# Performance work log

Measured on AMD Instinct MI355X. Metric: run time of the kernel, lower is better.

Reference implementation:

```python
import jax, jax.numpy as jnp
import numpy as np


def setup_inputs() -> dict:
    key = jax.random.key(0)
    ks = jax.random.split(key, 6)
    b, c, h, w = 8, 256, 48, 48
    return {
        "qry_fts": jax.random.normal(ks[0], (b, c, h, w), dtype=jnp.float32),
        "mask_fts": jax.random.normal(ks[1], (b, c, h, w), dtype=jnp.float32),
        "fts": jax.random.normal(ks[2], (b, c, h, w), dtype=jnp.float32),
        "Wq": jax.random.normal(ks[3], (c, c), dtype=jnp.float32) * (1.0 / np.sqrt(c)),
        "Wk": jax.random.normal(ks[4], (c, c), dtype=jnp.float32) * (1.0 / np.sqrt(c)),
        "Wv": jax.random.normal(ks[5], (c, c), dtype=jnp.float32) * (1.0 / np.sqrt(c)),
        "mu": jnp.full((1,), 0.5, dtype=jnp.float32),
    }


def reference(qry_fts, mask_fts, fts, Wq, Wk, Wv, mu):
    b, c, h, w = qry_fts.shape
    # flatten spatial dims to tokens: [b, N, c], N = h*w
    q_tok = qry_fts.reshape(b, c, h * w).transpose(0, 2, 1)
    m_tok = mask_fts.reshape(b, c, h * w).transpose(0, 2, 1)
    f_tok = fts.reshape(b, c, h * w).transpose(0, 2, 1)

    # torch Linear(no bias): y = x @ W^T with W [out,in]
    Q = jnp.einsum("bnc,dc->bnd", q_tok, Wq)
    K1 = jnp.einsum("bnc,dc->bnd", f_tok, Wk)
    K2 = jnp.einsum("bnc,dc->bnd", m_tok, Wk)
    V = jnp.einsum("bnc,dc->bnd", f_tok, Wv)

    A1 = jax.nn.softmax(jnp.einsum("bqd,bkd->bqk", Q, K1), axis=-1)
    A2 = jax.nn.softmax(jnp.einsum("bqd,bkd->bqk", Q, K2), axis=-1)
    A = (A1 * 0.5 + A2 * mu[0]) / (0.5 + mu[0])

    att = jnp.einsum("bqk,bkd->bqd", A, V)  # [b, N, c]
    att = att.reshape(b, h, w, c).transpose(0, 3, 1, 2)
    return qry_fts + att
```

## Files before the change

### kernel.cpp

```cpp
#include <hip/hip_runtime.h>
#include <math.h>

#define BB 8
#define CC 256
#define NTOK 2304
#define NPL 36
#define LOG2E 1.4426950408889634f
#define BIAS2 72.134752f

typedef __attribute__((ext_vector_type(4))) float f32x4;
typedef __attribute__((ext_vector_type(8))) short s16x8;
typedef __attribute__((ext_vector_type(4))) short s16x4;

__device__ inline unsigned short f2bf(float x) {
  unsigned u = __builtin_bit_cast(unsigned, x);
  return (unsigned short)((u + 0x7FFFu + ((u >> 16) & 1u)) >> 16);
}
__device__ inline float bf2f(unsigned short h) {
  return __builtin_bit_cast(float, (unsigned)h << 16);
}
__device__ inline unsigned short f2h(float x) {
  _Float16 h = (_Float16)x;
  return __builtin_bit_cast(unsigned short, h);
}

__device__ inline void async16(void* lds, const void* g) {
  __builtin_amdgcn_global_load_lds(
      (const __attribute__((address_space(1))) unsigned int*)g,
      (__attribute__((address_space(3))) unsigned int*)lds, 16, 0, 0);
}

__global__ __launch_bounds__(256)
void prep_kernel(const float* __restrict__ X0, const float* __restrict__ X1,
                 const float* __restrict__ X2, unsigned short* __restrict__ Y0,
                 unsigned short* __restrict__ Y1, unsigned short* __restrict__ Y2) {
  __shared__ float Ls[64][65];
  const int t = threadIdx.x;
  const int n0 = blockIdx.x * 64, c0 = blockIdx.y * 64;
  const int z = blockIdx.z, src = z >> 3, b = z & 7;
  const float* X = (src == 0) ? X0 : (src == 1) ? X1 : X2;
  unsigned short* Y = (src == 0) ? Y0 : (src == 1) ? Y1 : Y2;
  const float* Xb = X + (size_t)b * CC * NTOK;
  unsigned short* Yb = Y + (size_t)b * CC * NTOK;

  #pragma unroll
  for (int rr = 0; rr < 16; rr++) {
    int cl = rr * 4 + (t >> 6);
    Ls[cl][t & 63] = Xb[(size_t)(c0 + cl) * NTOK + n0 + (t & 63)];
  }
  __syncthreads();
  #pragma unroll
  for (int rr = 0; rr < 8; rr++) {
    int nl = rr * 8 + (t >> 5);
    int cl = (t & 31) * 2;
    unsigned v = (unsigned)f2h(Ls[cl][nl]) | ((unsigned)f2h(Ls[cl + 1][nl]) << 16);
    *(unsigned*)((char*)Yb + ((size_t)(n0 + nl) * CC + c0 + cl) * 2) = v;
  }
}

__global__ __launch_bounds__(256)
void wconv_kernel(const float* __restrict__ Wq, const float* __restrict__ Wk,
                  const float* __restrict__ Wv, unsigned short* __restrict__ Wqh,
                  unsigned short* __restrict__ Wkh, unsigned short* __restrict__ Wvh) {
  const float* src = (blockIdx.y == 0) ? Wq : (blockIdx.y == 1) ? Wk : Wv;
  unsigned short* dst = (blockIdx.y == 0) ? Wqh : (blockIdx.y == 1) ? Wkh : Wvh;
  int gi = (blockIdx.x * 256 + threadIdx.x) * 4;
  f32x4 v = *(const f32x4*)(src + gi);
  s16x4 o;
  #pragma unroll
  for (int i = 0; i < 4; i++) o[i] = (short)f2h(v[i]);
  *(s16x4*)(dst + gi) = o;
}

__global__ __launch_bounds__(256, 2)
void gemm_kernel(const unsigned short* __restrict__ Xtq, const unsigned short* __restrict__ Xtm,
                 const unsigned short* __restrict__ Xtf, const unsigned short* __restrict__ Wqh,
                 const unsigned short* __restrict__ Wkh, const unsigned short* __restrict__ Wvh,
                 unsigned short* __restrict__ Qw, unsigned short* __restrict__ K1w,
                 unsigned short* __restrict__ K2w, unsigned short* __restrict__ Vtw) {
  __shared__ alignas(16) char smem[32768];

  const int m = blockIdx.y;
  const unsigned short* Xt = (m == 0) ? Xtq : (m == 2) ? Xtm : Xtf;
  const unsigned short* Wh = (m == 0) ? Wqh : (m == 3) ? Wvh : Wkh;
  unsigned short* Y = (m == 0) ? Qw : (m == 1) ? K1w : (m == 2) ? K2w : Vtw;

  const int t = threadIdx.x;
  const int w = t >> 6, l = t & 63, g = l >> 4, c = l & 15;
  const int bid = blockIdx.x;
  const int b = bid & 7, nt = bid >> 3;
  const int n0w = nt * 64 + w * 16;
  const size_t bo = (size_t)b * CC * NTOK;

  const char* Xb = (const char*)(Xt + bo);
  const char* Wb = (const char*)Wh;
  char* Yb = (char*)(Y + bo);

  int koff[4], cdst[4];
  #pragma unroll
  for (int j = 0; j < 4; j++) {
    int ck = w + 4 * j;
    int row = ck * 2 + (l >> 5);
    koff[j] = row * 512 + (((l & 31) * 16) ^ ((row & 7) << 4));
    cdst[j] = ck * 1024 + l * 16;
  }
  int kxor[8];
  #pragma unroll
  for (int dc = 0; dc < 8; dc++)
    kxor[dc] = (dc * 64 + g * 16) ^ ((c & 7) << 4);

  s16x8 xa[8];
  #pragma unroll
  for (int dc = 0; dc < 8; dc++)
    xa[dc] = *(const s16x8*)(Xb + (n0w + c) * 512 + dc * 64 + g * 16);

  f32x4 acc[16];

#define STAGE_W(WB, TILE)                                            \
  do {                                                               \
    _Pragma("unroll")                                                \
    for (int j_ = 0; j_ < 4; j_++)                                   \
      async16((WB) + cdst[j_], Wb + (TILE) * 16384 + koff[j_]);      \
  } while (0)

  STAGE_W(smem, 0);
  __syncthreads();

  #pragma unroll
  for (int ph = 0; ph < 8; ph++) {
    char* cur = smem + (ph & 1) * 16384;
    if (ph < 7) STAGE_W(smem + ((ph & 1) ^ 1) * 16384, ph + 1);
    __builtin_amdgcn_s_setprio(1);
    #pragma unroll
    for (int s = 0; s < 2; s++) {
      const char* Kt = cur + (s * 16 + c) * 512;
      f32x4 sx[2] = {(f32x4){0.f, 0.f, 0.f, 0.f}, (f32x4){0.f, 0.f, 0.f, 0.f}};
      #pragma unroll
      for (int dc = 0; dc < 8; dc++) {
        s16x8 wf = *(const s16x8*)(Kt + kxor[dc]);
        sx[dc >> 2] = __builtin_amdgcn_mfma_f32_16x16x32_f16(xa[dc], wf, sx[dc >> 2], 0, 0, 0);
      }
      acc[ph * 2 + s] = sx[0] + sx[1];
    }
    __builtin_amdgcn_s_setprio(0);
    __syncthreads();
  }
#undef STAGE_W

  if (m != 3) {
    unsigned short* Ws = (unsigned short*)(smem + w * 8192);
    const float scale = (m == 0) ? LOG2E : 1.0f;
    #pragma unroll
    for (int dt = 0; dt < 16; dt++)
      #pragma unroll
      for (int j = 0; j < 4; j++)
        Ws[(g * 4 + j) * 256 + dt * 16 + c] = f2h(acc[dt][j] * scale);
    #pragma unroll
    for (int r = 0; r < 16; r++) {
      s16x4 v = *(const s16x4*)&Ws[r * 256 + l * 4];
      *(s16x4*)(Yb + (size_t)(n0w + r) * 512 + l * 8) = v;
    }
  } else {
    unsigned short* Vs = (unsigned short*)(smem + w * 8192);
    #pragma unroll
    for (int dt = 0; dt < 16; dt++) {
      s16x4 pv;
      #pragma unroll
      for (int j = 0; j < 4; j++) pv[j] = (short)f2bf(acc[dt][j]);
      *(s16x4*)&Vs[c * 20 + g * 4] = pv;
      s16x4 vv = *(const s16x4*)&Vs[(l >> 2) * 20 + (l & 3) * 4];
      *(s16x4*)(Yb + (size_t)(dt * 16 + (l >> 2)) * 4608 + (size_t)(n0w + (l & 3) * 4) * 2) = vv;
    }
  }
}

__global__ __launch_bounds__(256, 2)
void attn_kernel(const unsigned short* __restrict__ Qf, const unsigned short* __restrict__ K1,
                 const unsigned short* __restrict__ K2, const unsigned short* __restrict__ Vt,
                 unsigned short* __restrict__ pa1, unsigned short* __restrict__ pa2,
                 float* __restrict__ lb) {
  __shared__ alignas(16) char smem[77824];
  char* const kb0 = smem;
  char* const kb1 = smem + 16384;

  const int t = threadIdx.x;
  const int w = t >> 6, l = t & 63, g = l >> 4, c = l & 15;
  const int path = w >> 1, qs = w & 1;
  const int bid = blockIdx.x;
  const int b = bid & 7;
  const int r0 = bid >> 3;
  const int qt = r0 % 36, half = r0 / 36;
  const int q0 = qt * 64 + qs * 32;
  const size_t bo = (size_t)b * CC * NTOK;

  const char* Qb  = (const char*)(Qf + bo);
  const char* K1b = (const char*)(K1 + bo);
  const char* K2b = (const char*)(K2 + bo);
  const char* Vtb = (const char*)(Vt + bo);

  unsigned short* const Pe  = (unsigned short*)(smem + 65536 + w * 3072);
  unsigned short* const Pod = Pe + 768;

  int koff[2], voff[2], cdst[2];
  #pragma unroll
  for (int j = 0; j < 2; j++) {
    int ck = w + 4 * j;
    int tok = ck * 2 + (l >> 5);
    koff[j] = tok * 512 + (((l & 31) * 16) ^ ((tok & 7) << 4));
    voff[j] = (ck * 32 + (l >> 1)) * 4608 + (((l & 1) ^ ((l >> 3) & 1)) << 4);
    cdst[j] = ck * 1024 + l * 16;
  }

  int kxor[8];
  #pragma unroll
  for (int dc = 0; dc < 8; dc++)
    kxor[dc] = (dc * 64 + g * 16) ^ ((c & 7) << 4);

  s16x8 qf[2][8];
  #pragma unroll
  for (int st = 0; st < 2; st++)
    #pragma unroll
    for (int dc = 0; dc < 8; dc++)
      qf[st][dc] = *(const s16x8*)(Qb + (q0 + st * 16 + c) * 512 + dc * 64 + g * 16);

  f32x4 a0[16], a1r[16];
  #pragma unroll
  for (int dt = 0; dt < 16; dt++) {
    a0[dt]  = (f32x4){0.f, 0.f, 0.f, 0.f};
    a1r[dt] = (f32x4){0.f, 0.f, 0.f, 0.f};
  }
  float lr[2][4] = {{0.f, 0.f, 0.f, 0.f}, {0.f, 0.f, 0.f, 0.f}};

#define STAGE_K(KB, TILE)                                                  \
  do {                                                                     \
    _Pragma("unroll")                                                      \
    for (int pp_ = 0; pp_ < 2; pp_++) {                                    \
      const char* ks_ = (pp_ ? K2b : K1b) + (size_t)(TILE) * 8192;         \
      async16((KB) + pp_ * 8192 + cdst[0], ks_ + koff[0]);                 \
      async16((KB) + pp_ * 8192 + cdst[1], ks_ + koff[1]);                 \
    }                                                                      \
  } while (0)

#define STAGE_V(VB, PAIR)                                                  \
  do {                                                                     \
    _Pragma("unroll")                                                      \
    for (int h_ = 0; h_ < 2; h_++) {                                       \
      const char* vs_ = Vtb + (PAIR) * 64 + h_ * 32;                       \
      async16((VB) + h_ * 8192 + cdst[0], vs_ + voff[0]);                  \
      async16((VB) + h_ * 8192 + cdst[1], vs_ + voff[1]);                  \
    }                                                                      \
  } while (0)

  const int tb = half * 72;
  const int pb = half * 36;

  STAGE_K(kb0, tb);
  STAGE_V(smem + 32768, pb);
  __syncthreads();

  for (int p = 0; p < NPL; p++) {
    char* vcur = smem + 32768 + (p & 1) * 16384;
    char* vnxt = smem + 32768 + ((p & 1) ^ 1) * 16384;

    STAGE_K(kb1, tb + 2 * p + 1);
    {
      const char* Kt = kb0 + path * 8192 + c * 512;
      f32x4 s0 = (f32x4){0.f, 0.f, 0.f, 0.f};
      f32x4 s1 = (f32x4){0.f, 0.f, 0.f, 0.f};
      __builtin_amdgcn_s_setprio(1);
      #pragma unroll
      for (int dc = 0; dc < 8; dc++) {
        s16x8 kf = *(const s16x8*)(Kt + kxor[dc]);
        s0 = __builtin_amdgcn_mfma_f32_16x16x32_f16(qf[0][dc], kf, s0, 0, 0, 0);
        s1 = __builtin_amdgcn_mfma_f32_16x16x32_f16(qf[1][dc], kf, s1, 0, 0, 0);
      }
      __builtin_amdgcn_s_setprio(0);
      #pragma unroll
      for (int j = 0; j < 4; j++) {
        float pv = exp2f(s0[j] - BIAS2);
        lr[0][j] += pv;
        Pe[(g * 4 + j) * 24 + c] = f2bf(pv);
        float pw = exp2f(s1[j] - BIAS2);
        lr[1][j] += pw;
        Pe[(16 + g * 4 + j) * 24 + c] = f2bf(pw);
      }
    }
    __syncthreads();

    if (p + 1 < NPL) {
      STAGE_K(kb0, tb + 2 * p + 2);
      STAGE_V(vnxt, pb + p + 1);
    }
    {
      const char* Kt = kb1 + path * 8192 + c * 512;
      f32x4 s0 = (f32x4){0.f, 0.f, 0.f, 0.f};
      f32x4 s1 = (f32x4){0.f, 0.f, 0.f, 0.f};
      __builtin_amdgcn_s_setprio(1);
      #pragma unroll
      for (int dc = 0; dc < 8; dc++) {
        s16x8 kf = *(const s16x8*)(Kt + kxor[dc]);
        s0 = __builtin_amdgcn_mfma_f32_16x16x32_f16(qf[0][dc], kf, s0, 0, 0, 0);
        s1 = __builtin_amdgcn_mfma_f32_16x16x32_f16(qf[1][dc], kf, s1, 0, 0, 0);
      }
      __builtin_amdgcn_s_setprio(0);
      #pragma unroll
      for (int j = 0; j < 4; j++) {
        float pv = exp2f(s0[j] - BIAS2);
        lr[0][j] += pv;
        Pod[(g * 4 + j) * 24 + c] = f2bf(pv);
        float pw = exp2f(s1[j] - BIAS2);
        lr[1][j] += pw;
        Pod[(16 + g * 4 + j) * 24 + c] = f2bf(pw);
      }
    }
    {
      s16x8 pa0 = *(const s16x8*)(((g < 2) ? Pe : Pod) + (c) * 24 + (g & 1) * 8);
      s16x8 pa1 = *(const s16x8*)(((g < 2) ? Pe : Pod) + (16 + c) * 24 + (g & 1) * 8);
      const char* vbase = vcur + ((g >= 2) ? 8192 : 0) + c * 32 +
                          ((((g & 1) ^ ((c >> 2) & 1))) << 4);
      __builtin_amdgcn_s_setprio(1);
      #pragma unroll
      for (int dt = 0; dt < 16; dt++) {
        s16x8 vf = *(const s16x8*)(vbase + dt * 512);
        a0[dt]  = __builtin_amdgcn_mfma_f32_16x16x32_bf16(pa0, vf, a0[dt], 0, 0, 0);
        a1r[dt] = __builtin_amdgcn_mfma_f32_16x16x32_bf16(pa1, vf, a1r[dt], 0, 0, 0);
      }
      __builtin_amdgcn_s_setprio(0);
    }
    __syncthreads();
  }
#undef STAGE_K
#undef STAGE_V

  #pragma unroll
  for (int st = 0; st < 2; st++)
    #pragma unroll
    for (int j = 0; j < 4; j++) {
      #pragma unroll
      for (int off = 1; off < 16; off <<= 1)
        lr[st][j] += __shfl_xor(lr[st][j], off);
    }
  const int pqidx = (half * 8 + b) * 36 + qt;
  if (c == 0) {
    #pragma unroll
    for (int st = 0; st < 2; st++)
      #pragma unroll
      for (int j = 0; j < 4; j++)
        lb[path * 36864 + pqidx * 64 + qs * 32 + st * 16 + g * 4 + j] = lr[st][j];
  }

  unsigned short* const pdst = (path ? pa2 : pa1) + (size_t)pqidx * 16384;
  float* Ws = (float*)(smem + w * 4352);
  const int q = l & 15, ds = l >> 4;
  #pragma unroll
  for (int st = 0; st < 2; st++) {
    const f32x4* ap = st ? a1r : a0;
    #pragma unroll
    for (int ch = 0; ch < 4; ch++) {
      #pragma unroll
      for (int dtp = 0; dtp < 4; dtp++) {
        const int dt = ch * 4 + dtp;
        #pragma unroll
        for (int j = 0; j < 4; j++)
          Ws[(g * 4 + j) * 68 + dtp * 16 + c] = ap[dt][j];
      }
      #pragma unroll
      for (int i = 0; i < 16; i++) {
        int d = ch * 64 + i * 4 + ds;
        pdst[d * 64 + qs * 32 + st * 16 + q] = f2bf(Ws[q * 68 + i * 4 + ds]);
      }
    }
  }
}

__global__ __launch_bounds__(256)
void combine_kernel(const unsigned short* __restrict__ pa1, const unsigned short* __restrict__ pa2,
                    const float* __restrict__ lb, const float* __restrict__ qry,
                    const float* __restrict__ mup, float* __restrict__ out) {
  const int bid = blockIdx.x;
  const int b = bid & 7, qt = bid >> 3;
  const int t = threadIdx.x;
  const int q = t & 63, dr = t >> 6;
  const size_t bo = (size_t)b * CC * NTOK;
  const int q0 = qt * 64;

  const int i0 = (0 * 8 + b) * 36 + qt;
  const int i1 = (1 * 8 + b) * 36 + qt;
  float l1 = lb[i0 * 64 + q] + lb[i1 * 64 + q];
  float l2 = lb[36864 + i0 * 64 + q] + lb[36864 + i1 * 64 + q];
  const float mu = mup[0];
  const float w1 = 0.5f / (0.5f + mu) / l1;
  const float w2 = mu / (0.5f + mu) / l2;

  const unsigned short* p10 = pa1 + (size_t)i0 * 16384;
  const unsigned short* p11 = pa1 + (size_t)i1 * 16384;
  const unsigned short* p20 = pa2 + (size_t)i0 * 16384;
  const unsigned short* p21 = pa2 + (size_t)i1 * 16384;

  #pragma unroll
  for (int i = 0; i < 64; i++) {
    int d = dr * 64 + i;
    int off = d * 64 + q;
    float av1 = bf2f(p10[off]) + bf2f(p11[off]);
    float av2 = bf2f(p20[off]) + bf2f(p21[off]);
    size_t gi = bo + (size_t)d * NTOK + q0 + q;
    out[gi] = qry[gi] + av1 * w1 + av2 * w2;
  }
}

extern "C" void kernel_launch(void* const* d_in, const int* in_sizes, int n_in,
                              void* d_out, int out_size, void* d_ws, size_t ws_size,
                              hipStream_t stream) {
  const float* qry  = (const float*)d_in[0];
  const float* mask = (const float*)d_in[1];
  const float* fts  = (const float*)d_in[2];
  const float* Wq   = (const float*)d_in[3];
  const float* Wk   = (const float*)d_in[4];
  const float* Wv   = (const float*)d_in[5];
  const float* mu   = (const float*)d_in[6];
  float* out = (float*)d_out;

  const size_t SZ = (size_t)BB * CC * NTOK;
  unsigned short* base = (unsigned short*)d_ws;
  unsigned short* PA1 = base;
  unsigned short* PA2 = base + 9437184;
  float*          LB  = (float*)(base + 18874368);
  unsigned short* Xtq = base;
  unsigned short* Xtm = base + SZ;
  unsigned short* Xtf = base + 2 * SZ;
  unsigned short* Qw  = base + 19169280;
  unsigned short* K1w = Qw + SZ;
  unsigned short* K2w = Qw + 2 * SZ;
  unsigned short* Vtw = Qw + 3 * SZ;
  unsigned short* Wqh = Qw + 4 * SZ;
  unsigned short* Wkh = Wqh + CC * CC;
  unsigned short* Wvh = Wkh + CC * CC;

  prep_kernel<<<dim3(NTOK / 64, CC / 64, 24), 256, 0, stream>>>(qry, mask, fts, Xtq, Xtm, Xtf);
  wconv_kernel<<<dim3(64, 3), 256, 0, stream>>>(Wq, Wk, Wv, Wqh, Wkh, Wvh);

  const int GG = BB * (NTOK / 64);
  gemm_kernel<<<dim3(GG, 4), 256, 0, stream>>>(Xtq, Xtm, Xtf, Wqh, Wkh, Wvh,
                                               Qw, K1w, K2w, Vtw);

  attn_kernel<<<2 * GG, 256, 0, stream>>>(Qw, K1w, K2w, Vtw, PA1, PA2, LB);
  combine_kernel<<<GG, 256, 0, stream>>>(PA1, PA2, LB, qry, mu, out);
}
```

Baseline: 229.2 us.

## Fuse weight conversion into prep and combine into attention via arrival counters

Weight fp16 conversion now runs in an extra z-slice of the prep kernel, so there is one fewer launch. The separate combine kernel is removed. The second of the two split-KV attention blocks for each query tile, detected through an atomic arrival counter, performs the normalization and residual add. This cuts launch overhead and the kernel boundary before combine, but adds a memset launch, thread fences and tail work inside the attention kernel.

```diff
diff --git a/kernel.cpp b/kernel.cpp
--- a/kernel.cpp
+++ b/kernel.cpp
@@ -33,11 +33,31 @@
 __global__ __launch_bounds__(256)
 void prep_kernel(const float* __restrict__ X0, const float* __restrict__ X1,
                  const float* __restrict__ X2, unsigned short* __restrict__ Y0,
-                 unsigned short* __restrict__ Y1, unsigned short* __restrict__ Y2) {
+                 unsigned short* __restrict__ Y1, unsigned short* __restrict__ Y2,
+                 const float* __restrict__ W0, const float* __restrict__ W1,
+                 const float* __restrict__ W2, unsigned short* __restrict__ Wh0,
+                 unsigned short* __restrict__ Wh1, unsigned short* __restrict__ Wh2) {
   __shared__ float Ls[64][65];
   const int t = threadIdx.x;
+  const int z = blockIdx.z;
+
+  if (z == 24) {
+    int idx = (blockIdx.x * 4 + blockIdx.y) * 256 + t;
+    for (int e = idx; e < 49152; e += 36864) {
+      int m = e / 16384, r = e - m * 16384;
+      const float* s = (m == 0) ? W0 : (m == 1) ? W1 : W2;
+      unsigned short* d = (m == 0) ? Wh0 : (m == 1) ? Wh1 : Wh2;
+      f32x4 v = *(const f32x4*)(s + r * 4);
+      s16x4 o;
+      #pragma unroll
+      for (int i = 0; i < 4; i++) o[i] = (short)f2h(v[i]);
+      *(s16x4*)(d + r * 4) = o;
+    }
+    return;
+  }
+
   const int n0 = blockIdx.x * 64, c0 = blockIdx.y * 64;
-  const int z = blockIdx.z, src = z >> 3, b = z & 7;
+  const int src = z >> 3, b = z & 7;
   const float* X = (src == 0) ? X0 : (src == 1) ? X1 : X2;
   unsigned short* Y = (src == 0) ? Y0 : (src == 1) ? Y1 : Y2;
   const float* Xb = X + (size_t)b * CC * NTOK;
@@ -56,20 +76,6 @@
     unsigned v = (unsigned)f2h(Ls[cl][nl]) | ((unsigned)f2h(Ls[cl + 1][nl]) << 16);
     *(unsigned*)((char*)Yb + ((size_t)(n0 + nl) * CC + c0 + cl) * 2) = v;
   }
-}
-
-__global__ __launch_bounds__(256)
-void wconv_kernel(const float* __restrict__ Wq, const float* __restrict__ Wk,
-                  const float* __restrict__ Wv, unsigned short* __restrict__ Wqh,
-                  unsigned short* __restrict__ Wkh, unsigned short* __restrict__ Wvh) {
-  const float* src = (blockIdx.y == 0) ? Wq : (blockIdx.y == 1) ? Wk : Wv;
-  unsigned short* dst = (blockIdx.y == 0) ? Wqh : (blockIdx.y == 1) ? Wkh : Wvh;
-  int gi = (blockIdx.x * 256 + threadIdx.x) * 4;
-  f32x4 v = *(const f32x4*)(src + gi);
-  s16x4 o;
-  #pragma unroll
-  for (int i = 0; i < 4; i++) o[i] = (short)f2h(v[i]);
-  *(s16x4*)(dst + gi) = o;
 }
 
 __global__ __launch_bounds__(256, 2)
@@ -178,7 +184,9 @@
 void attn_kernel(const unsigned short* __restrict__ Qf, const unsigned short* __restrict__ K1,
                  const unsigned short* __restrict__ K2, const unsigned short* __restrict__ Vt,
                  unsigned short* __restrict__ pa1, unsigned short* __restrict__ pa2,
-                 float* __restrict__ lb) {
+                 float* __restrict__ lb, int* __restrict__ flags,
+                 const float* __restrict__ qry, const float* __restrict__ mup,
+                 float* __restrict__ out) {
   __shared__ alignas(16) char smem[77824];
   char* const kb0 = smem;
   char* const kb1 = smem + 16384;
@@ -371,40 +379,36 @@
       }
     }
   }
-}
-
-__global__ __launch_bounds__(256)
-void combine_kernel(const unsigned short* __restrict__ pa1, const unsigned short* __restrict__ pa2,
-                    const float* __restrict__ lb, const float* __restrict__ qry,
-                    const float* __restrict__ mup, float* __restrict__ out) {
-  const int bid = blockIdx.x;
-  const int b = bid & 7, qt = bid >> 3;
-  const int t = threadIdx.x;
-  const int q = t & 63, dr = t >> 6;
-  const size_t bo = (size_t)b * CC * NTOK;
-  const int q0 = qt * 64;
-
-  const int i0 = (0 * 8 + b) * 36 + qt;
-  const int i1 = (1 * 8 + b) * 36 + qt;
-  float l1 = lb[i0 * 64 + q] + lb[i1 * 64 + q];
-  float l2 = lb[36864 + i0 * 64 + q] + lb[36864 + i1 * 64 + q];
-  const float mu = mup[0];
-  const float w1 = 0.5f / (0.5f + mu) / l1;
-  const float w2 = mu / (0.5f + mu) / l2;
-
-  const unsigned short* p10 = pa1 + (size_t)i0 * 16384;
-  const unsigned short* p11 = pa1 + (size_t)i1 * 16384;
-  const unsigned short* p20 = pa2 + (size_t)i0 * 16384;
-  const unsigned short* p21 = pa2 + (size_t)i1 * 16384;
-
-  #pragma unroll
-  for (int i = 0; i < 64; i++) {
-    int d = dr * 64 + i;
-    int off = d * 64 + q;
-    float av1 = bf2f(p10[off]) + bf2f(p11[off]);
-    float av2 = bf2f(p20[off]) + bf2f(p21[off]);
-    size_t gi = bo + (size_t)d * NTOK + q0 + q;
-    out[gi] = qry[gi] + av1 * w1 + av2 * w2;
+
+  __threadfence();
+  __syncthreads();
+  __shared__ int arriver;
+  if (t == 0) arriver = atomicAdd(&flags[b * 36 + qt], 1);
+  __syncthreads();
+  if (arriver == 1) {
+    __threadfence();
+    const int cq = t & 63, dr = t >> 6;
+    const int i0 = b * 36 + qt;
+    const int i1 = 288 + b * 36 + qt;
+    float l1 = lb[i0 * 64 + cq] + lb[i1 * 64 + cq];
+    float l2 = lb[36864 + i0 * 64 + cq] + lb[36864 + i1 * 64 + cq];
+    const float muv = mup[0];
+    const float w1 = 0.5f / (0.5f + muv) / l1;
+    const float w2 = muv / (0.5f + muv) / l2;
+    const unsigned short* p10 = pa1 + (size_t)i0 * 16384;
+    const unsigned short* p11 = pa1 + (size_t)i1 * 16384;
+    const unsigned short* p20 = pa2 + (size_t)i0 * 16384;
+    const unsigned short* p21 = pa2 + (size_t)i1 * 16384;
+    const int qg = qt * 64;
+    #pragma unroll
+    for (int i = 0; i < 64; i++) {
+      int d = dr * 64 + i;
+      int off = d * 64 + cq;
+      float av1 = bf2f(p10[off]) + bf2f(p11[off]);
+      float av2 = bf2f(p20[off]) + bf2f(p21[off]);
+      size_t gi = bo + (size_t)d * NTOK + qg + cq;
+      out[gi] = qry[gi] + av1 * w1 + av2 * w2;
+    }
   }
 }
 
@@ -435,14 +439,17 @@
   unsigned short* Wqh = Qw + 4 * SZ;
   unsigned short* Wkh = Wqh + CC * CC;
   unsigned short* Wvh = Wkh + CC * CC;
-
-  prep_kernel<<<dim3(NTOK / 64, CC / 64, 24), 256, 0, stream>>>(qry, mask, fts, Xtq, Xtm, Xtf);
-  wconv_kernel<<<dim3(64, 3), 256, 0, stream>>>(Wq, Wk, Wv, Wqh, Wkh, Wvh);
+  int*            FLAGS = (int*)(Wvh + CC * CC);
+
+  hipMemsetAsync(FLAGS, 0, 288 * sizeof(int), stream);
+
+  prep_kernel<<<dim3(NTOK / 64, CC / 64, 25), 256, 0, stream>>>(
+      qry, mask, fts, Xtq, Xtm, Xtf, Wq, Wk, Wv, Wqh, Wkh, Wvh);
 
   const int GG = BB * (NTOK / 64);
   gemm_kernel<<<dim3(GG, 4), 256, 0, stream>>>(Xtq, Xtm, Xtf, Wqh, Wkh, Wvh,
                                                Qw, K1w, K2w, Vtw);
 
-  attn_kernel<<<2 * GG, 256, 0, stream>>>(Qw, K1w, K2w, Vtw, PA1, PA2, LB);
-  combine_kernel<<<GG, 256, 0, stream>>>(PA1, PA2, LB, qry, mu, out);
-}
+  attn_kernel<<<2 * GG, 256, 0, stream>>>(Qw, K1w, K2w, Vtw, PA1, PA2, LB,
+                                          FLAGS, qry, mu, out);
+}
```

After: 371.9 us. +62.3%, slower.
